# Kernel tuning notes

Measured on AMD Instinct MI355X. Metric: run time of the kernel, lower is better.

The kernel has to match this reference:

```python
import jax, jax.numpy as jnp
import numpy as np

GAMMA = 0.99
CLIP_VALUE = 5.0
B, T = 4096, 4096


def setup_inputs() -> dict:
    key = jax.random.key(0)
    k1, k2, k3, k4 = jax.random.split(key, 4)
    return {
        "log_probs": jax.random.normal(k1, (B, T), dtype=jnp.float32),
        "logits": jax.random.normal(k2, (B, T), dtype=jnp.float32),
        "weight": jax.random.uniform(k3, (B, T), dtype=jnp.float32),
        "baselines": jax.random.normal(k4, (B, T), dtype=jnp.float32),
    }


def _discounted_reverse_cumsum(wr):
    # wr: [B, T]. c[t] = wr[t] + GAMMA * c[t+1]  (reverse linear recurrence)
    def step(carry, x):
        c = x + GAMMA * carry
        return c, c
    # scan over time, reversed; xs shape [T, B]
    _, cs = jax.lax.scan(step, jnp.zeros(wr.shape[0], wr.dtype), wr.T, reverse=True)
    return cs.T  # [B, T]


def reference(log_probs, logits, weight, baselines):
    rewards = jax.nn.log_sigmoid(logits)                    # [B, T]
    cumulative_rewards = _discounted_reverse_cumsum(weight * rewards)
    advantages = cumulative_rewards - baselines
    advantages = advantages - advantages.mean(axis=0)       # center over batch
    advantages = jnp.clip(advantages, -CLIP_VALUE, CLIP_VALUE)
    generator_objective = (advantages * log_probs).sum(axis=1)  # [B]
    return generator_objective, cumulative_rewards
```

## Files before the change

### kernel.cpp

```cpp
#include <hip/hip_runtime.h>
#include <math.h>

#define B_DIM 4096
#define T_DIM 4096

constexpr float GAMMA_F = 0.99f;
constexpr float CLIP_V  = 5.0f;

constexpr float G2    = GAMMA_F * GAMMA_F;
constexpr float G4    = G2 * G2;
constexpr float G8    = G4 * G4;
constexpr float Q1    = G8 * G8;
constexpr float Q2    = Q1 * Q1;
constexpr float Q4    = Q2 * Q2;
constexpr float Q8    = Q4 * Q4;
constexpr float Q16   = Q8 * Q8;
constexpr float Q32   = Q16 * Q16;
constexpr float G1024 = Q32 * Q32;

__device__ __forceinline__ float pow_g4(int e) {
    float f = 1.0f;
    if (e & 1)  f *= G4;
    if (e & 2)  f *= G8;
    if (e & 4)  f *= Q1;
    if (e & 8)  f *= Q2;
    if (e & 16) f *= Q4;
    if (e & 32) f *= Q8;
    return f;
}

__device__ __forceinline__ float lsig(float x) {
    return fminf(x, 0.0f) - __logf(1.0f + __expf(-fabsf(x)));
}

__global__ __launch_bounds__(256) void k_scan(const float4* __restrict__ logits,
                                              const float4* __restrict__ weight,
                                              float4* __restrict__ cum) {
    __shared__ float waveS[4];
    const int row = blockIdx.x;
    const int tid = threadIdx.x;
    const int wv = tid >> 6, ln = tid & 63;
    const size_t rb  = (size_t)row * (T_DIM / 4);
    const int    seg = wv * 256 + ln;

    float wr[16];
    #pragma unroll
    for (int j = 0; j < 4; ++j) {
        float4 x4 = logits[rb + seg + j * 64];
        float4 w4 = weight[rb + seg + j * 64];
        wr[4 * j + 0] = w4.x * lsig(x4.x);
        wr[4 * j + 1] = w4.y * lsig(x4.y);
        wr[4 * j + 2] = w4.z * lsig(x4.z);
        wr[4 * j + 3] = w4.w * lsig(x4.w);
    }

    float t[4], sn[4];
    const float F4[6] = {G4, G8, Q1, Q2, Q4, Q8};
    #pragma unroll
    for (int j = 0; j < 4; ++j) {
        float V = 0.0f;
        #pragma unroll
        for (int i = 3; i >= 0; --i) V = fmaf(GAMMA_F, V, wr[4 * j + i]);
        float s = V;
        #pragma unroll
        for (int k = 0; k < 6; ++k) {
            int off = 1 << k;
            float u = __shfl_down(s, off, 64);
            if (ln + off < 64) s = fmaf(F4[k], u, s);
        }
        float nx = __shfl_down(s, 1, 64);
        sn[j] = (ln == 63) ? 0.0f : nx;
        t[j]  = __shfl(s, 0, 64);
    }

    float W = fmaf(Q16, fmaf(Q16, fmaf(Q16, t[3], t[2]), t[1]), t[0]);
    if (ln == 0) waveS[wv] = W;
    __syncthreads();

    float Anext = 0.0f;
    for (int w2 = 3; w2 > wv; --w2) Anext = fmaf(G1024, Anext, waveS[w2]);

    float U[5];
    U[4] = Anext;
    #pragma unroll
    for (int j = 3; j >= 1; --j) U[j] = fmaf(Q16, U[j + 1], t[j]);

    const float fac = pow_g4(63 - ln);

    #pragma unroll
    for (int j = 0; j < 4; ++j) {
        float carry = fmaf(fac, U[j + 1], sn[j]);
        float4 o4;
        o4.w = carry = fmaf(GAMMA_F, carry, wr[4 * j + 3]);
        o4.z = carry = fmaf(GAMMA_F, carry, wr[4 * j + 2]);
        o4.y = carry = fmaf(GAMMA_F, carry, wr[4 * j + 1]);
        o4.x = carry = fmaf(GAMMA_F, carry, wr[4 * j + 0]);
        cum[rb + seg + j * 64] = o4;
    }
}

__global__ __launch_bounds__(256) void k_zero(float* __restrict__ p) {
    p[blockIdx.x * 256 + threadIdx.x] = 0.0f;
}

__global__ __launch_bounds__(256) void k_colsum(const float* __restrict__ cum,
                                                const float* __restrict__ baselines,
                                                float* __restrict__ colsum) {
    const int t = blockIdx.x * 256 + threadIdx.x;
    size_t p = (size_t)(blockIdx.y * 32) * T_DIM + t;
    float s0 = 0.0f, s1 = 0.0f, s2 = 0.0f, s3 = 0.0f;
    #pragma unroll
    for (int r = 0; r < 32; r += 4) {
        s0 += cum[p] - baselines[p];               p += T_DIM;
        s1 += cum[p] - baselines[p];               p += T_DIM;
        s2 += cum[p] - baselines[p];               p += T_DIM;
        s3 += cum[p] - baselines[p];               p += T_DIM;
    }
    atomicAdd(&colsum[t], (s0 + s1) + (s2 + s3));
}

__global__ __launch_bounds__(256) void k_obj(const float4* __restrict__ cum,
                                             const float4* __restrict__ baselines,
                                             const float4* __restrict__ logp,
                                             const float4* __restrict__ colsum,
                                             float* __restrict__ obj) {
    constexpr float invB = 1.0f / B_DIM;
    const int row = blockIdx.x, tid = threadIdx.x;
    const size_t base4 = (size_t)row * (T_DIM / 4);
    float acc = 0.0f;
    #pragma unroll
    for (int j = 0; j < 4; ++j) {
        int t4 = j * 256 + tid;
        float4 c = cum[base4 + t4];
        float4 b = baselines[base4 + t4];
        float4 l = logp[base4 + t4];
        float4 m = colsum[t4];
        float a0 = fminf(fmaxf(c.x - b.x - m.x * invB, -CLIP_V), CLIP_V);
        float a1 = fminf(fmaxf(c.y - b.y - m.y * invB, -CLIP_V), CLIP_V);
        float a2 = fminf(fmaxf(c.z - b.z - m.z * invB, -CLIP_V), CLIP_V);
        float a3 = fminf(fmaxf(c.w - b.w - m.w * invB, -CLIP_V), CLIP_V);
        acc = fmaf(a0, l.x, acc);
        acc = fmaf(a1, l.y, acc);
        acc = fmaf(a2, l.z, acc);
        acc = fmaf(a3, l.w, acc);
    }
    #pragma unroll
    for (int off = 32; off > 0; off >>= 1) acc += __shfl_down(acc, off, 64);
    __shared__ float ws4[4];
    if ((tid & 63) == 0) ws4[tid >> 6] = acc;
    __syncthreads();
    if (tid == 0) obj[row] = (ws4[0] + ws4[1]) + (ws4[2] + ws4[3]);
}

extern "C" void kernel_launch(void* const* d_in, const int* in_sizes, int n_in,
                              void* d_out, int out_size, void* d_ws, size_t ws_size,
                              hipStream_t stream) {
    const float* log_probs = (const float*)d_in[0];
    const float* logits    = (const float*)d_in[1];
    const float* weight    = (const float*)d_in[2];
    const float* baselines = (const float*)d_in[3];

    float* obj = (float*)d_out;
    float* cum = obj + B_DIM;
    float* colsum = (float*)d_ws;

    k_zero  <<<T_DIM / 256, 256, 0, stream>>>(colsum);
    k_scan  <<<B_DIM, 256, 0, stream>>>((const float4*)logits, (const float4*)weight,
                                        (float4*)cum);
    k_colsum<<<dim3(T_DIM / 256, 128), 256, 0, stream>>>(cum, baselines, colsum);
    k_obj   <<<B_DIM, 256, 0, stream>>>((const float4*)cum, (const float4*)baselines,
                                        (const float4*)log_probs, (const float4*)colsum, obj);
}
```

Before: 281.4 us.

## Fuse scan, column sum and objective into one cooperative persistent kernel

Replaces the four-kernel pipeline with a single cooperative kernel. Each block handles four rows and keeps the baseline-subtracted advantages in registers, so cum and baselines are not re-read. Grid-wide syncs separate the zeroing, the column-sum atomics and the objective pass, and the old path remains as a fallback if cooperative launch fails. The cost is two grid barriers, heavy register pressure from holding four rows of advantages, and a grid of 1024 blocks that must all be co-resident for the cooperative launch to succeed.

```diff
diff --git a/kernel.cpp b/kernel.cpp
--- a/kernel.cpp
+++ b/kernel.cpp
@@ -1,8 +1,13 @@
 #include <hip/hip_runtime.h>
+#include <hip/hip_cooperative_groups.h>
 #include <math.h>
+
+namespace cg = cooperative_groups;
 
 #define B_DIM 4096
 #define T_DIM 4096
+#define ROWS  4
+#define GRID  (B_DIM / ROWS)
 
 constexpr float GAMMA_F = 0.99f;
 constexpr float CLIP_V  = 5.0f;
@@ -33,6 +38,137 @@
     return fminf(x, 0.0f) - __logf(1.0f + __expf(-fabsf(x)));
 }
 
+__global__ __launch_bounds__(256, 4) void k_fused(
+        const float4* __restrict__ logits, const float4* __restrict__ weight,
+        const float4* __restrict__ baselines, const float4* __restrict__ logp,
+        float* __restrict__ obj, float4* __restrict__ cum,
+        float* __restrict__ colsum) {
+    cg::grid_group grid = cg::this_grid();
+    __shared__ float waveS[ROWS][4];
+    __shared__ float red[ROWS][4];
+
+    const int bid = blockIdx.x, tid = threadIdx.x;
+    const int wv = tid >> 6, ln = tid & 63;
+    const int seg = wv * 256 + ln;
+
+    if (bid < 16) colsum[bid * 256 + tid] = 0.0f;
+    __threadfence();
+    grid.sync();
+
+    const float F4[6] = {G4, G8, Q1, Q2, Q4, Q8};
+    float4 adv[ROWS][4];
+
+    #pragma unroll
+    for (int r = 0; r < ROWS; ++r) {
+        const int row = bid * ROWS + r;
+        const size_t rb = (size_t)row * (T_DIM / 4);
+        float wr[16];
+        #pragma unroll
+        for (int j = 0; j < 4; ++j) {
+            float4 x4 = logits[rb + seg + j * 64];
+            float4 w4 = weight[rb + seg + j * 64];
+            wr[4 * j + 0] = w4.x * lsig(x4.x);
+            wr[4 * j + 1] = w4.y * lsig(x4.y);
+            wr[4 * j + 2] = w4.z * lsig(x4.z);
+            wr[4 * j + 3] = w4.w * lsig(x4.w);
+        }
+        float t[4], sn[4];
+        #pragma unroll
+        for (int j = 0; j < 4; ++j) {
+            float V = 0.0f;
+            #pragma unroll
+            for (int i = 3; i >= 0; --i) V = fmaf(GAMMA_F, V, wr[4 * j + i]);
+            float s = V;
+            #pragma unroll
+            for (int k = 0; k < 6; ++k) {
+                int off = 1 << k;
+                float u = __shfl_down(s, off, 64);
+                if (ln + off < 64) s = fmaf(F4[k], u, s);
+            }
+            float nx = __shfl_down(s, 1, 64);
+            sn[j] = (ln == 63) ? 0.0f : nx;
+            t[j]  = __shfl(s, 0, 64);
+        }
+        float W = fmaf(Q16, fmaf(Q16, fmaf(Q16, t[3], t[2]), t[1]), t[0]);
+        if (ln == 0) waveS[r][wv] = W;
+        __syncthreads();
+        float Anext = 0.0f;
+        for (int w2 = 3; w2 > wv; --w2) Anext = fmaf(G1024, Anext, waveS[r][w2]);
+        float U[5];
+        U[4] = Anext;
+        #pragma unroll
+        for (int j = 3; j >= 1; --j) U[j] = fmaf(Q16, U[j + 1], t[j]);
+        const float fac = pow_g4(63 - ln);
+        #pragma unroll
+        for (int j = 0; j < 4; ++j) {
+            float carry = fmaf(fac, U[j + 1], sn[j]);
+            float4 o4;
+            o4.w = carry = fmaf(GAMMA_F, carry, wr[4 * j + 3]);
+            o4.z = carry = fmaf(GAMMA_F, carry, wr[4 * j + 2]);
+            o4.y = carry = fmaf(GAMMA_F, carry, wr[4 * j + 1]);
+            o4.x = carry = fmaf(GAMMA_F, carry, wr[4 * j + 0]);
+            cum[rb + seg + j * 64] = o4;
+            float4 b4 = baselines[rb + seg + j * 64];
+            adv[r][j] = make_float4(o4.x - b4.x, o4.y - b4.y,
+                                    o4.z - b4.z, o4.w - b4.w);
+        }
+    }
+
+    #pragma unroll
+    for (int j = 0; j < 4; ++j) {
+        const int c = 4 * (seg + j * 64);
+        atomicAdd(&colsum[c + 0], (adv[0][j].x + adv[1][j].x) + (adv[2][j].x + adv[3][j].x));
+        atomicAdd(&colsum[c + 1], (adv[0][j].y + adv[1][j].y) + (adv[2][j].y + adv[3][j].y));
+        atomicAdd(&colsum[c + 2], (adv[0][j].z + adv[1][j].z) + (adv[2][j].z + adv[3][j].z));
+        atomicAdd(&colsum[c + 3], (adv[0][j].w + adv[1][j].w) + (adv[2][j].w + adv[3][j].w));
+    }
+    grid.sync();
+    __threadfence();
+
+    constexpr float invB = 1.0f / B_DIM;
+    float m[4][4];
+    #pragma unroll
+    for (int j = 0; j < 4; ++j) {
+        const int c = 4 * (seg + j * 64);
+        #pragma unroll
+        for (int i = 0; i < 4; ++i)
+            m[j][i] = invB * __hip_atomic_load(&colsum[c + i], __ATOMIC_RELAXED,
+                                               __HIP_MEMORY_SCOPE_AGENT);
+    }
+    float acc[ROWS];
+    #pragma unroll
+    for (int r = 0; r < ROWS; ++r) {
+        const size_t rb = (size_t)(bid * ROWS + r) * (T_DIM / 4);
+        float a = 0.0f;
+        #pragma unroll
+        for (int j = 0; j < 4; ++j) {
+            float4 l4 = logp[rb + seg + j * 64];
+            float4 v  = adv[r][j];
+            float a0 = fminf(fmaxf(v.x - m[j][0], -CLIP_V), CLIP_V);
+            float a1 = fminf(fmaxf(v.y - m[j][1], -CLIP_V), CLIP_V);
+            float a2 = fminf(fmaxf(v.z - m[j][2], -CLIP_V), CLIP_V);
+            float a3 = fminf(fmaxf(v.w - m[j][3], -CLIP_V), CLIP_V);
+            a = fmaf(a0, l4.x, a);
+            a = fmaf(a1, l4.y, a);
+            a = fmaf(a2, l4.z, a);
+            a = fmaf(a3, l4.w, a);
+        }
+        acc[r] = a;
+    }
+    #pragma unroll
+    for (int off = 32; off > 0; off >>= 1) {
+        #pragma unroll
+        for (int r = 0; r < ROWS; ++r) acc[r] += __shfl_down(acc[r], off, 64);
+    }
+    if (ln == 0) {
+        #pragma unroll
+        for (int r = 0; r < ROWS; ++r) red[r][wv] = acc[r];
+    }
+    __syncthreads();
+    if (tid < ROWS)
+        obj[bid * ROWS + tid] = (red[tid][0] + red[tid][1]) + (red[tid][2] + red[tid][3]);
+}
+
 __global__ __launch_bounds__(256) void k_scan(const float4* __restrict__ logits,
                                               const float4* __restrict__ weight,
                                               float4* __restrict__ cum) {
@@ -53,7 +189,6 @@
         wr[4 * j + 2] = w4.z * lsig(x4.z);
         wr[4 * j + 3] = w4.w * lsig(x4.w);
     }
-
     float t[4], sn[4];
     const float F4[6] = {G4, G8, Q1, Q2, Q4, Q8};
     #pragma unroll
@@ -72,21 +207,16 @@
         sn[j] = (ln == 63) ? 0.0f : nx;
         t[j]  = __shfl(s, 0, 64);
     }
-
     float W = fmaf(Q16, fmaf(Q16, fmaf(Q16, t[3], t[2]), t[1]), t[0]);
     if (ln == 0) waveS[wv] = W;
     __syncthreads();
-
     float Anext = 0.0f;
     for (int w2 = 3; w2 > wv; --w2) Anext = fmaf(G1024, Anext, waveS[w2]);
-
     float U[5];
     U[4] = Anext;
     #pragma unroll
     for (int j = 3; j >= 1; --j) U[j] = fmaf(Q16, U[j + 1], t[j]);
-
     const float fac = pow_g4(63 - ln);
-
     #pragma unroll
     for (int j = 0; j < 4; ++j) {
         float carry = fmaf(fac, U[j + 1], sn[j]);
@@ -160,9 +290,29 @@
     const float* weight    = (const float*)d_in[2];
     const float* baselines = (const float*)d_in[3];
 
-    float* obj = (float*)d_out;
-    float* cum = obj + B_DIM;
+    float* obj    = (float*)d_out;
+    float* cum    = obj + B_DIM;
     float* colsum = (float*)d_ws;
+
+    static int coop = -1;
+    if (coop < 0) {
+        int v = 0;
+        hipDeviceGetAttribute(&v, hipDeviceAttributeCooperativeLaunch, 0);
+        coop = v;
+    }
+    if (coop) {
+        const float4* lg4 = (const float4*)logits;
+        const float4* wt4 = (const float4*)weight;
+        const float4* bs4 = (const float4*)baselines;
+        const float4* lp4 = (const float4*)log_probs;
+        float4*       cm4 = (float4*)cum;
+        void* args[] = {(void*)&lg4, (void*)&wt4, (void*)&bs4, (void*)&lp4,
+                        (void*)&obj, (void*)&cm4, (void*)&colsum};
+        hipError_t rc = hipLaunchCooperativeKernel((const void*)k_fused,
+                                                   dim3(GRID), dim3(256),
+                                                   args, 0, stream);
+        if (rc == hipSuccess) return;
+    }
 
     k_zero  <<<T_DIM / 256, 256, 0, stream>>>(colsum);
     k_scan  <<<B_DIM, 256, 0, stream>>>((const float4*)logits, (const float4*)weight,
```

After: 578.8 us. 106% more time.

## Fuse baseline column partial sums into scan kernel with two rows per block

Applied to the files above, without the earlier changes.

The scan kernel now handles two rows per block. It reads baselines alongside the scan outputs and accumulates per-block column partial sums of (cum - baselines) into a workspace buffer. A separate reduction kernel then folds these partials into colsum with atomics. The aim is to avoid re-reading cum and baselines in a dedicated column-sum pass, at the cost of writing and re-reading a partials buffer of roughly 32 MB. The old path is kept as a fallback when the workspace is too small.

```diff
diff --git a/kernel.cpp b/kernel.cpp
--- a/kernel.cpp
+++ b/kernel.cpp
@@ -3,6 +3,9 @@
 
 #define B_DIM 4096
 #define T_DIM 4096
+#define ROWS  2
+#define NSCAN (B_DIM / ROWS)
+#define CG    64
 
 constexpr float GAMMA_F = 0.99f;
 constexpr float CLIP_V  = 5.0f;
@@ -33,90 +36,103 @@
     return fminf(x, 0.0f) - __logf(1.0f + __expf(-fabsf(x)));
 }
 
-__global__ __launch_bounds__(256) void k_scan(const float4* __restrict__ logits,
-                                              const float4* __restrict__ weight,
-                                              float4* __restrict__ cum) {
+__global__ __launch_bounds__(256) void k_scan_cs(
+        const float4* __restrict__ logits, const float4* __restrict__ weight,
+        const float4* __restrict__ baselines, float4* __restrict__ cum,
+        float4* __restrict__ partials) {
     __shared__ float waveS[4];
-    const int row = blockIdx.x;
-    const int tid = threadIdx.x;
+    const int bid = blockIdx.x, tid = threadIdx.x;
     const int wv = tid >> 6, ln = tid & 63;
-    const size_t rb  = (size_t)row * (T_DIM / 4);
-    const int    seg = wv * 256 + ln;
-
-    float wr[16];
-    #pragma unroll
-    for (int j = 0; j < 4; ++j) {
-        float4 x4 = logits[rb + seg + j * 64];
-        float4 w4 = weight[rb + seg + j * 64];
-        wr[4 * j + 0] = w4.x * lsig(x4.x);
-        wr[4 * j + 1] = w4.y * lsig(x4.y);
-        wr[4 * j + 2] = w4.z * lsig(x4.z);
-        wr[4 * j + 3] = w4.w * lsig(x4.w);
-    }
-
-    float t[4], sn[4];
+    const int seg = wv * 256 + ln;
     const float F4[6] = {G4, G8, Q1, Q2, Q4, Q8};
-    #pragma unroll
-    for (int j = 0; j < 4; ++j) {
-        float V = 0.0f;
-        #pragma unroll
-        for (int i = 3; i >= 0; --i) V = fmaf(GAMMA_F, V, wr[4 * j + i]);
-        float s = V;
-        #pragma unroll
-        for (int k = 0; k < 6; ++k) {
-            int off = 1 << k;
-            float u = __shfl_down(s, off, 64);
-            if (ln + off < 64) s = fmaf(F4[k], u, s);
-        }
-        float nx = __shfl_down(s, 1, 64);
-        sn[j] = (ln == 63) ? 0.0f : nx;
-        t[j]  = __shfl(s, 0, 64);
-    }
-
-    float W = fmaf(Q16, fmaf(Q16, fmaf(Q16, t[3], t[2]), t[1]), t[0]);
-    if (ln == 0) waveS[wv] = W;
-    __syncthreads();
-
-    float Anext = 0.0f;
-    for (int w2 = 3; w2 > wv; --w2) Anext = fmaf(G1024, Anext, waveS[w2]);
-
-    float U[5];
-    U[4] = Anext;
-    #pragma unroll
-    for (int j = 3; j >= 1; --j) U[j] = fmaf(Q16, U[j + 1], t[j]);
-
-    const float fac = pow_g4(63 - ln);
-
-    #pragma unroll
-    for (int j = 0; j < 4; ++j) {
-        float carry = fmaf(fac, U[j + 1], sn[j]);
-        float4 o4;
-        o4.w = carry = fmaf(GAMMA_F, carry, wr[4 * j + 3]);
-        o4.z = carry = fmaf(GAMMA_F, carry, wr[4 * j + 2]);
-        o4.y = carry = fmaf(GAMMA_F, carry, wr[4 * j + 1]);
-        o4.x = carry = fmaf(GAMMA_F, carry, wr[4 * j + 0]);
-        cum[rb + seg + j * 64] = o4;
-    }
+
+    float4 colacc[4];
+    #pragma unroll
+    for (int j = 0; j < 4; ++j) colacc[j] = make_float4(0.f, 0.f, 0.f, 0.f);
+
+    #pragma unroll 1
+    for (int r = 0; r < ROWS; ++r) {
+        const size_t rb = (size_t)(bid * ROWS + r) * (T_DIM / 4);
+
+        float wr[16];
+        #pragma unroll
+        for (int j = 0; j < 4; ++j) {
+            float4 x4 = logits[rb + seg + j * 64];
+            float4 w4 = weight[rb + seg + j * 64];
+            wr[4 * j + 0] = w4.x * lsig(x4.x);
+            wr[4 * j + 1] = w4.y * lsig(x4.y);
+            wr[4 * j + 2] = w4.z * lsig(x4.z);
+            wr[4 * j + 3] = w4.w * lsig(x4.w);
+        }
+
+        float t[4], sn[4];
+        #pragma unroll
+        for (int j = 0; j < 4; ++j) {
+            float V = 0.0f;
+            #pragma unroll
+            for (int i = 3; i >= 0; --i) V = fmaf(GAMMA_F, V, wr[4 * j + i]);
+            float s = V;
+            #pragma unroll
+            for (int k = 0; k < 6; ++k) {
+                int off = 1 << k;
+                float u = __shfl_down(s, off, 64);
+                if (ln + off < 64) s = fmaf(F4[k], u, s);
+            }
+            float nx = __shfl_down(s, 1, 64);
+            sn[j] = (ln == 63) ? 0.0f : nx;
+            t[j]  = __shfl(s, 0, 64);
+        }
+        float W = fmaf(Q16, fmaf(Q16, fmaf(Q16, t[3], t[2]), t[1]), t[0]);
+        if (r) __syncthreads();
+        if (ln == 0) waveS[wv] = W;
+        __syncthreads();
+        float Anext = 0.0f;
+        for (int w2 = 3; w2 > wv; --w2) Anext = fmaf(G1024, Anext, waveS[w2]);
+        float U[5];
+        U[4] = Anext;
+        #pragma unroll
+        for (int j = 3; j >= 1; --j) U[j] = fmaf(Q16, U[j + 1], t[j]);
+        const float fac = pow_g4(63 - ln);
+
+        #pragma unroll
+        for (int j = 0; j < 4; ++j) {
+            float carry = fmaf(fac, U[j + 1], sn[j]);
+            float4 o4;
+            o4.w = carry = fmaf(GAMMA_F, carry, wr[4 * j + 3]);
+            o4.z = carry = fmaf(GAMMA_F, carry, wr[4 * j + 2]);
+            o4.y = carry = fmaf(GAMMA_F, carry, wr[4 * j + 1]);
+            o4.x = carry = fmaf(GAMMA_F, carry, wr[4 * j + 0]);
+            cum[rb + seg + j * 64] = o4;
+            float4 b4 = baselines[rb + seg + j * 64];
+            colacc[j].x += o4.x - b4.x;
+            colacc[j].y += o4.y - b4.y;
+            colacc[j].z += o4.z - b4.z;
+            colacc[j].w += o4.w - b4.w;
+        }
+    }
+
+    #pragma unroll
+    for (int j = 0; j < 4; ++j)
+        partials[(size_t)bid * (T_DIM / 4) + seg + j * 64] = colacc[j];
 }
 
 __global__ __launch_bounds__(256) void k_zero(float* __restrict__ p) {
     p[blockIdx.x * 256 + threadIdx.x] = 0.0f;
 }
 
-__global__ __launch_bounds__(256) void k_colsum(const float* __restrict__ cum,
-                                                const float* __restrict__ baselines,
+__global__ __launch_bounds__(256) void k_colred(const float* __restrict__ partials,
                                                 float* __restrict__ colsum) {
-    const int t = blockIdx.x * 256 + threadIdx.x;
-    size_t p = (size_t)(blockIdx.y * 32) * T_DIM + t;
+    const int col = blockIdx.x * 256 + threadIdx.x;
+    size_t p = (size_t)blockIdx.y * CG * T_DIM + col;
     float s0 = 0.0f, s1 = 0.0f, s2 = 0.0f, s3 = 0.0f;
-    #pragma unroll
-    for (int r = 0; r < 32; r += 4) {
-        s0 += cum[p] - baselines[p];               p += T_DIM;
-        s1 += cum[p] - baselines[p];               p += T_DIM;
-        s2 += cum[p] - baselines[p];               p += T_DIM;
-        s3 += cum[p] - baselines[p];               p += T_DIM;
-    }
-    atomicAdd(&colsum[t], (s0 + s1) + (s2 + s3));
+    #pragma unroll 4
+    for (int i = 0; i < CG; i += 4) {
+        s0 += partials[p];  p += T_DIM;
+        s1 += partials[p];  p += T_DIM;
+        s2 += partials[p];  p += T_DIM;
+        s3 += partials[p];  p += T_DIM;
+    }
+    atomicAdd(&colsum[col], (s0 + s1) + (s2 + s3));
 }
 
 __global__ __launch_bounds__(256) void k_obj(const float4* __restrict__ cum,
@@ -152,6 +168,82 @@
     if (tid == 0) obj[row] = (ws4[0] + ws4[1]) + (ws4[2] + ws4[3]);
 }
 
+__global__ __launch_bounds__(256) void k_scan(const float4* __restrict__ logits,
+                                              const float4* __restrict__ weight,
+                                              float4* __restrict__ cum) {
+    __shared__ float waveS[4];
+    const int row = blockIdx.x;
+    const int tid = threadIdx.x;
+    const int wv = tid >> 6, ln = tid & 63;
+    const size_t rb  = (size_t)row * (T_DIM / 4);
+    const int    seg = wv * 256 + ln;
+
+    float wr[16];
+    #pragma unroll
+    for (int j = 0; j < 4; ++j) {
+        float4 x4 = logits[rb + seg + j * 64];
+        float4 w4 = weight[rb + seg + j * 64];
+        wr[4 * j + 0] = w4.x * lsig(x4.x);
+        wr[4 * j + 1] = w4.y * lsig(x4.y);
+        wr[4 * j + 2] = w4.z * lsig(x4.z);
+        wr[4 * j + 3] = w4.w * lsig(x4.w);
+    }
+    float t[4], sn[4];
+    const float F4[6] = {G4, G8, Q1, Q2, Q4, Q8};
+    #pragma unroll
+    for (int j = 0; j < 4; ++j) {
+        float V = 0.0f;
+        #pragma unroll
+        for (int i = 3; i >= 0; --i) V = fmaf(GAMMA_F, V, wr[4 * j + i]);
+        float s = V;
+        #pragma unroll
+        for (int k = 0; k < 6; ++k) {
+            int off = 1 << k;
+            float u = __shfl_down(s, off, 64);
+            if (ln + off < 64) s = fmaf(F4[k], u, s);
+        }
+        float nx = __shfl_down(s, 1, 64);
+        sn[j] = (ln == 63) ? 0.0f : nx;
+        t[j]  = __shfl(s, 0, 64);
+    }
+    float W = fmaf(Q16, fmaf(Q16, fmaf(Q16, t[3], t[2]), t[1]), t[0]);
+    if (ln == 0) waveS[wv] = W;
+    __syncthreads();
+    float Anext = 0.0f;
+    for (int w2 = 3; w2 > wv; --w2) Anext = fmaf(G1024, Anext, waveS[w2]);
+    float U[5];
+    U[4] = Anext;
+    #pragma unroll
+    for (int j = 3; j >= 1; --j) U[j] = fmaf(Q16, U[j + 1], t[j]);
+    const float fac = pow_g4(63 - ln);
+    #pragma unroll
+    for (int j = 0; j < 4; ++j) {
+        float carry = fmaf(fac, U[j + 1], sn[j]);
+        float4 o4;
+        o4.w = carry = fmaf(GAMMA_F, carry, wr[4 * j + 3]);
+        o4.z = carry = fmaf(GAMMA_F, carry, wr[4 * j + 2]);
+        o4.y = carry = fmaf(GAMMA_F, carry, wr[4 * j + 1]);
+        o4.x = carry = fmaf(GAMMA_F, carry, wr[4 * j + 0]);
+        cum[rb + seg + j * 64] = o4;
+    }
+}
+
+__global__ __launch_bounds__(256) void k_colsum(const float* __restrict__ cum,
+                                                const float* __restrict__ baselines,
+                                                float* __restrict__ colsum) {
+    const int t = blockIdx.x * 256 + threadIdx.x;
+    size_t p = (size_t)(blockIdx.y * 32) * T_DIM + t;
+    float s0 = 0.0f, s1 = 0.0f, s2 = 0.0f, s3 = 0.0f;
+    #pragma unroll
+    for (int r = 0; r < 32; r += 4) {
+        s0 += cum[p] - baselines[p];               p += T_DIM;
+        s1 += cum[p] - baselines[p];               p += T_DIM;
+        s2 += cum[p] - baselines[p];               p += T_DIM;
+        s3 += cum[p] - baselines[p];               p += T_DIM;
+    }
+    atomicAdd(&colsum[t], (s0 + s1) + (s2 + s3));
+}
+
 extern "C" void kernel_launch(void* const* d_in, const int* in_sizes, int n_in,
                               void* d_out, int out_size, void* d_ws, size_t ws_size,
                               hipStream_t stream) {
@@ -160,14 +252,32 @@
     const float* weight    = (const float*)d_in[2];
     const float* baselines = (const float*)d_in[3];
 
-    float* obj = (float*)d_out;
-    float* cum = obj + B_DIM;
+    float* obj    = (float*)d_out;
+    float* cum    = obj + B_DIM;
     float* colsum = (float*)d_ws;
-
-    k_zero  <<<T_DIM / 256, 256, 0, stream>>>(colsum);
-    k_scan  <<<B_DIM, 256, 0, stream>>>((const float4*)logits, (const float4*)weight,
-                                        (float4*)cum);
-    k_colsum<<<dim3(T_DIM / 256, 128), 256, 0, stream>>>(cum, baselines, colsum);
-    k_obj   <<<B_DIM, 256, 0, stream>>>((const float4*)cum, (const float4*)baselines,
-                                        (const float4*)log_probs, (const float4*)colsum, obj);
-}
+    float* partials = colsum + T_DIM;
+
+    const size_t need = (size_t)T_DIM * 4 + (size_t)NSCAN * T_DIM * 4;
+
+    if (ws_size >= need) {
+        k_zero   <<<T_DIM / 256, 256, 0, stream>>>(colsum);
+        k_scan_cs<<<NSCAN, 256, 0, stream>>>((const float4*)logits,
+                                             (const float4*)weight,
+                                             (const float4*)baselines,
+                                             (float4*)cum, (float4*)partials);
+        k_colred <<<dim3(T_DIM / 256, NSCAN / CG), 256, 0, stream>>>(partials, colsum);
+        k_obj    <<<B_DIM, 256, 0, stream>>>((const float4*)cum,
+                                             (const float4*)baselines,
+                                             (const float4*)log_probs,
+                                             (const float4*)colsum, obj);
+    } else {
+        k_zero  <<<T_DIM / 256, 256, 0, stream>>>(colsum);
+        k_scan  <<<B_DIM, 256, 0, stream>>>((const float4*)logits,
+                                            (const float4*)weight, (float4*)cum);
+        k_colsum<<<dim3(T_DIM / 256, 128), 256, 0, stream>>>(cum, baselines, colsum);
+        k_obj   <<<B_DIM, 256, 0, stream>>>((const float4*)cum,
+                                            (const float4*)baselines,
+                                            (const float4*)log_probs,
+                                            (const float4*)colsum, obj);
+    }
+}
```

Result: slower. 287.5 us (+2.2%).
